# Kernel optimization log

Measured on AMD Instinct MI355X. Metric: run time of the kernel, lower is better.

Reference implementation:

```python
import jax, jax.numpy as jnp
import numpy as np


def setup_inputs() -> dict:
    key = jax.random.key(0)
    kq, kk, kv = jax.random.split(key, 3)
    B, S, D = 4, 4096, 64
    q = jax.random.normal(kq, (B, S, D), dtype=jnp.float32)
    k = jax.random.normal(kk, (B, S, D), dtype=jnp.float32)
    v = jax.random.normal(kv, (B, S, D), dtype=jnp.float32)
    return {"q": q, "k": k, "v": v}


def reference(q, k, v):
    # Faithful math of the original blocked loop:
    #   output_i += exp(Q_i @ K_j^T) @ V_j, summed over all column blocks j
    # which is exactly unnormalized exponential attention:
    #   out = exp(Q K^T) V  (no 1/sqrt(d) scaling, no softmax normalization,
    #   no max-subtraction -- matching the source module's math).
    scores = jnp.einsum("bqd,bkd->bqk", q, k)  # [B, Sq, Sk]
    return jnp.einsum("bqk,bkd->bqd", jnp.exp(scores), v)  # [B, Sq, D]
```

## Files before the change

### kernel.cpp

```cpp
#include <hip/hip_runtime.h>
#include <hip/hip_bf16.h>


typedef short    s16x4 __attribute__((ext_vector_type(4)));
typedef short    s16x8 __attribute__((ext_vector_type(8)));
typedef _Float16 h16x8 __attribute__((ext_vector_type(8)));
typedef float    fx4   __attribute__((ext_vector_type(4)));
typedef float    fx16  __attribute__((ext_vector_type(16)));

constexpr int S = 4096, D = 64, BN = 128;
constexpr int QROWS = 128;
constexpr int TILES = S / BN;
constexpr int HALF_TILES = TILES / 2;
constexpr int TILE_SHORTS  = 16 * 512;
constexpr int BATCH_SHORTS = TILES * TILE_SHORTS;

__device__ __forceinline__ unsigned short f2bf(float x) {
    unsigned u = __float_as_uint(x);
    u = (u + 0x7FFFu + ((u >> 16) & 1u)) >> 16;
    return (unsigned short)u;
}
__device__ __forceinline__ float bf2f(unsigned short h) {
    return __uint_as_float(((unsigned)h) << 16);
}
__device__ __forceinline__ unsigned short f2h(float x) {
    union { _Float16 h; unsigned short s; } u;
    u.h = (_Float16)x;
    return u.s;
}
__device__ __forceinline__ unsigned pack_bf16(float lo, float hi) {
    __hip_bfloat162 r = __float22bfloat162_rn(make_float2(lo, hi));
    union { __hip_bfloat162 b; unsigned u; } c;
    c.b = r;
    return c.u;
}
__device__ __forceinline__ float ex2(float x) {
#if __has_builtin(__builtin_amdgcn_exp2f)
    return __builtin_amdgcn_exp2f(x);
#else
    return exp2f(x);
#endif
}

__global__ __launch_bounds__(256) void prep2(
    const float* __restrict__ k, const float* __restrict__ v,
    unsigned short* __restrict__ kf, unsigned short* __restrict__ vf)
{
    __shared__ unsigned short tile[128 * 72];
    const int tid   = threadIdx.x;
    const int which = blockIdx.x & 1;
    const int t     = (blockIdx.x >> 1) & 31;
    const int b     = blockIdx.x >> 6;
    const float* src = (which ? v : k) + ((size_t)b * S + t * BN) * D;

    #pragma unroll
    for (int i = 0; i < 8; ++i) {
        int f   = i * 256 + tid;
        int row = f >> 4;
        int c4  = (f & 15) << 2;
        float4 x = *(const float4*)(src + row * D + c4);
        s16x4 o;
        if (which) o = (s16x4){(short)f2bf(x.x), (short)f2bf(x.y),
                               (short)f2bf(x.z), (short)f2bf(x.w)};
        else       o = (s16x4){(short)f2h(x.x), (short)f2h(x.y),
                               (short)f2h(x.z), (short)f2h(x.w)};
        *(s16x4*)&tile[row * 72 + c4] = o;
    }
    __syncthreads();

    const int lane = tid & 63;
    unsigned short* dst = (which ? vf : kf) + (size_t)b * BATCH_SHORTS + t * TILE_SHORTS;
    #pragma unroll
    for (int i = 0; i < 4; ++i) {
        int c = (tid >> 6) * 4 + i;
        s16x8 o;
        if (which == 0) {
            int row = (c >> 2) * 32 + (lane & 31);
            int dc  = (c & 3) * 16 + (lane >> 5) * 8;
            o = *(const s16x8*)&tile[row * 72 + dc];
        } else {
            int r0 = (c >> 1) * 16 + (lane >> 5) * 8;
            int dc = (c & 1) * 32 + (lane & 31);
            #pragma unroll
            for (int j = 0; j < 8; ++j) o[j] = (short)tile[(r0 + j) * 72 + dc];
        }
        *(s16x8*)(dst + c * 512 + lane * 8) = o;
    }
}

__global__ __launch_bounds__(512, 2) void attn_main4(
    const float* __restrict__ q, const unsigned short* __restrict__ kf,
    const unsigned short* __restrict__ vf, float* __restrict__ partial)
{
    __shared__ unsigned short smem[3 * 2 * TILE_SHORTS];

    const int tid = threadIdx.x, lane = tid & 63, w = tid >> 6;
    const int h = lane >> 5, m5 = lane & 31;
    const int mh = w & 1, kkq = w >> 1;
    const int bid = blockIdx.x;
    const int slice = bid & 7;
    const int b = slice >> 1;
    const int kh = slice & 1;
    const int q0 = (bid >> 3) * QROWS;
    const int t0 = kh * HALF_TILES;

    const unsigned short* kfb = kf + (size_t)b * BATCH_SHORTS;
    const unsigned short* vfb = vf + (size_t)b * BATCH_SHORTS;

    const float LOG2E = 1.4426950408889634f;
    h16x8 qf[2][4];
    #pragma unroll
    for (int mt = 0; mt < 2; ++mt) {
        const float* qrow = q + ((size_t)b * S + q0 + mh * 64 + mt * 32 + m5) * D + h * 8;
        #pragma unroll
        for (int ks = 0; ks < 4; ++ks) {
            float4 a = *(const float4*)(qrow + ks * 16);
            float4 c = *(const float4*)(qrow + ks * 16 + 4);
            qf[mt][ks] = (h16x8){
                (_Float16)(a.x * LOG2E), (_Float16)(a.y * LOG2E),
                (_Float16)(a.z * LOG2E), (_Float16)(a.w * LOG2E),
                (_Float16)(c.x * LOG2E), (_Float16)(c.y * LOG2E),
                (_Float16)(c.z * LOG2E), (_Float16)(c.w * LOG2E)};
        }
    }

    fx16 oacc[2][2] = {};

    auto issue = [&](int t, int bi) {
        unsigned short* base = &smem[bi * 2 * TILE_SHORTS];
        #pragma unroll
        for (int ii = 0; ii < 4; ++ii) {
            int c = (ii & 1) * 8 + w;
            const unsigned short* g = (ii < 2 ? kfb : vfb)
                + (size_t)t * TILE_SHORTS + c * 512 + lane * 8;
            unsigned short* l = base + (ii < 2 ? 0 : TILE_SHORTS) + c * 512 + lane * 8;
            __builtin_amdgcn_global_load_lds(
                (const __attribute__((address_space(1))) unsigned int*)g,
                (__attribute__((address_space(3))) unsigned int*)l, 16, 0, 0);
        }
    };

    issue(t0 + 0, 0);
    issue(t0 + 1, 1);

    for (int i = 0; i < HALF_TILES; ++i) {
        const int bi = i % 3;
        __asm__ volatile("" ::: "memory");
        if (i + 1 < HALF_TILES) {
            __builtin_amdgcn_s_waitcnt(0x0F74);
        } else {
            __builtin_amdgcn_s_waitcnt(0x0F70);
        }
        __builtin_amdgcn_s_barrier();
        __asm__ volatile("" ::: "memory");
        if (i + 2 < HALF_TILES) issue(t0 + i + 2, (i + 2) % 3);

        const unsigned short* kb = &smem[bi * 2 * TILE_SHORTS];
        const unsigned short* vb = kb + TILE_SHORTS;

        fx16 sa[2] = {};
        #pragma unroll
        for (int ks = 0; ks < 4; ++ks) {
            h16x8 a = *(const h16x8*)(kb + (kkq * 4 + ks) * 512 + lane * 8);
            #pragma unroll
            for (int mt = 0; mt < 2; ++mt)
                sa[mt] = __builtin_amdgcn_mfma_f32_32x32x16_f16(a, qf[mt][ks], sa[mt], 0, 0, 0);
        }

        unsigned p01[2][8];
        #pragma unroll
        for (int mt = 0; mt < 2; ++mt)
            #pragma unroll
            for (int rp = 0; rp < 8; ++rp)
                p01[mt][rp] = pack_bf16(ex2(sa[mt][2 * rp]), ex2(sa[mt][2 * rp + 1]));

        union frag { unsigned u[4]; s16x8 v; };
        frag A[2][2];
        #pragma unroll
        for (int mt = 0; mt < 2; ++mt) {
#if __has_builtin(__builtin_amdgcn_permlane32_swap)
            typedef unsigned uix2 __attribute__((ext_vector_type(2)));
            uix2 r0 = __builtin_amdgcn_permlane32_swap(p01[mt][0], p01[mt][2], false, false);
            uix2 r1 = __builtin_amdgcn_permlane32_swap(p01[mt][1], p01[mt][3], false, false);
            A[mt][0].u[0] = r0.x; A[mt][0].u[1] = r1.x;
            A[mt][0].u[2] = r0.y; A[mt][0].u[3] = r1.y;
            uix2 r2 = __builtin_amdgcn_permlane32_swap(p01[mt][4], p01[mt][6], false, false);
            uix2 r3 = __builtin_amdgcn_permlane32_swap(p01[mt][5], p01[mt][7], false, false);
            A[mt][1].u[0] = r2.x; A[mt][1].u[1] = r3.x;
            A[mt][1].u[2] = r2.y; A[mt][1].u[3] = r3.y;
#else
            unsigned sw[8];
            #pragma unroll
            for (int rp = 0; rp < 8; ++rp)
                sw[rp] = (unsigned)__shfl_xor((int)p01[mt][rp], 32, 64);
            A[mt][0].u[0] = h ? sw[2]        : p01[mt][0];
            A[mt][0].u[1] = h ? sw[3]        : p01[mt][1];
            A[mt][0].u[2] = h ? p01[mt][2]   : sw[0];
            A[mt][0].u[3] = h ? p01[mt][3]   : sw[1];
            A[mt][1].u[0] = h ? sw[6]        : p01[mt][4];
            A[mt][1].u[1] = h ? sw[7]        : p01[mt][5];
            A[mt][1].u[2] = h ? p01[mt][6]   : sw[4];
            A[mt][1].u[3] = h ? p01[mt][7]   : sw[5];
#endif
        }

        #pragma unroll
        for (int u = 0; u < 2; ++u) {
            int ss = kkq * 2 + u;
            #pragma unroll
            for (int dt = 0; dt < 2; ++dt) {
                s16x8 vv = *(const s16x8*)(vb + (ss * 2 + dt) * 512 + lane * 8);
                #pragma unroll
                for (int mt = 0; mt < 2; ++mt)
                    oacc[mt][dt] = __builtin_amdgcn_mfma_f32_32x32x16_bf16(
                        A[mt][u].v, vv, oacc[mt][dt], 0, 0, 0);
            }
        }
    }

    __syncthreads();
    float* scratch = (float*)smem;
    float* pout = partial + ((size_t)kh * 4 + b) * S * D;
    #pragma unroll
    for (int dt = 0; dt < 2; ++dt) {
        if (kkq > 0) {
            float* dst = scratch + (size_t)(mh * 3 + (kkq - 1)) * 2048;
            #pragma unroll
            for (int mt = 0; mt < 2; ++mt)
                #pragma unroll
                for (int r = 0; r < 16; ++r)
                    dst[(mt * 16 + r) * 64 + lane] = oacc[mt][dt][r];
        }
        __syncthreads();
        if (kkq == 0) {
            #pragma unroll
            for (int mt = 0; mt < 2; ++mt)
                #pragma unroll
                for (int r = 0; r < 16; ++r) {
                    float val = oacc[mt][dt][r];
                    #pragma unroll
                    for (int p = 0; p < 3; ++p)
                        val += scratch[(size_t)(mh * 3 + p) * 2048 + (mt * 16 + r) * 64 + lane];
                    int row = q0 + mh * 64 + mt * 32 + (r & 3) + 8 * (r >> 2) + 4 * h;
                    pout[(size_t)row * D + dt * 32 + m5] = val;
                }
        }
        __syncthreads();
    }
}

__global__ __launch_bounds__(256) void reduce_out(
    const float4* __restrict__ p0, const float4* __restrict__ p1,
    float4* __restrict__ o, int n4)
{
    int i = blockIdx.x * 256 + threadIdx.x;
    if (i < n4) {
        float4 a = p0[i], b = p1[i];
        o[i] = make_float4(a.x + b.x, a.y + b.y, a.z + b.z, a.w + b.w);
    }
}

__global__ __launch_bounds__(1024) void attn_fallback(
    const float* __restrict__ q, const float* __restrict__ k,
    const float* __restrict__ v, float* __restrict__ out)
{
    __shared__ unsigned short Kh[64][72];
    __shared__ unsigned short Kl[64][72];
    __shared__ unsigned short Vt[64][68];
    __shared__ unsigned short Pf[64][72];

    const int tid = threadIdx.x, lane = tid & 63, wave = tid >> 6;
    const int quad = lane >> 4, tq = lane & 15;
    const int kkb = wave & 3, mba = wave >> 2;
    const int b = blockIdx.y, q0 = blockIdx.x * 64;
    const float* qb = q + (size_t)b * S * D;
    const float* kb = k + (size_t)b * S * D;
    const float* vb = v + (size_t)b * S * D;
    float* ob = out + (size_t)b * S * D;

    s16x8 qh[2], ql[2];
    {
        const float* qrow = qb + (size_t)(q0 + mba * 16 + tq) * D;
        #pragma unroll
        for (int ks = 0; ks < 2; ++ks) {
            const float* src = qrow + ks * 32 + quad * 8;
            float4 f0 = *(const float4*)src;
            float4 f1 = *(const float4*)(src + 4);
            float f[8] = {f0.x, f0.y, f0.z, f0.w, f1.x, f1.y, f1.z, f1.w};
            #pragma unroll
            for (int j = 0; j < 8; ++j) {
                unsigned short hh = f2bf(f[j]);
                qh[ks][j] = (short)hh;
                ql[ks][j] = (short)f2bf(f[j] - bf2f(hh));
            }
        }
    }
    fx4 oacc = {0.f, 0.f, 0.f, 0.f};
    const int krow = tid >> 4, kc4 = (tid & 15) << 2;
    const int vd = tid & 63, vk = (tid >> 6) << 2;

    for (int t = 0; t < S / 64; ++t) {
        __syncthreads();
        const float* kt = kb + (size_t)(t * 64 + krow) * D;
        const float* vt = vb + (size_t)(t * 64 + vk) * D;
        {
            float4 kv = *(const float4*)(kt + kc4);
            unsigned short h0 = f2bf(kv.x), h1 = f2bf(kv.y), h2 = f2bf(kv.z), h3 = f2bf(kv.w);
            s16x4 a = {(short)h0, (short)h1, (short)h2, (short)h3};
            s16x4 l4 = {(short)f2bf(kv.x - bf2f(h0)), (short)f2bf(kv.y - bf2f(h1)),
                        (short)f2bf(kv.z - bf2f(h2)), (short)f2bf(kv.w - bf2f(h3))};
            *(s16x4*)&Kh[krow][kc4] = a;
            *(s16x4*)&Kl[krow][kc4] = l4;
            const float* vs = vt + vd;
            s16x4 vv = {(short)f2bf(vs[0]), (short)f2bf(vs[D]),
                        (short)f2bf(vs[2 * D]), (short)f2bf(vs[3 * D])};
            *(s16x4*)&Vt[vd][vk] = vv;
        }
        __syncthreads();
        fx4 sacc = {0.f, 0.f, 0.f, 0.f};
        #pragma unroll
        for (int ks = 0; ks < 2; ++ks) {
            s16x8 kah = *(const s16x8*)&Kh[kkb * 16 + tq][ks * 32 + quad * 8];
            s16x8 kal = *(const s16x8*)&Kl[kkb * 16 + tq][ks * 32 + quad * 8];
            sacc = __builtin_amdgcn_mfma_f32_16x16x32_bf16(kah, qh[ks], sacc, 0, 0, 0);
            sacc = __builtin_amdgcn_mfma_f32_16x16x32_bf16(kah, ql[ks], sacc, 0, 0, 0);
            sacc = __builtin_amdgcn_mfma_f32_16x16x32_bf16(kal, qh[ks], sacc, 0, 0, 0);
        }
        s16x4 pp = {(short)f2bf(__expf(sacc[0])), (short)f2bf(__expf(sacc[1])),
                    (short)f2bf(__expf(sacc[2])), (short)f2bf(__expf(sacc[3]))};
        *(s16x4*)&Pf[mba * 16 + tq][kkb * 16 + (quad << 2)] = pp;
        __syncthreads();
        #pragma unroll
        for (int ks = 0; ks < 2; ++ks) {
            s16x8 pa = *(const s16x8*)&Pf[mba * 16 + tq][ks * 32 + quad * 8];
            const unsigned short* vr = &Vt[kkb * 16 + tq][ks * 32 + quad * 8];
            s16x4 va = *(const s16x4*)vr;
            s16x4 vb2 = *(const s16x4*)(vr + 4);
            s16x8 vfull = __builtin_shufflevector(va, vb2, 0, 1, 2, 3, 4, 5, 6, 7);
            oacc = __builtin_amdgcn_mfma_f32_16x16x32_bf16(pa, vfull, oacc, 0, 0, 0);
        }
    }
    #pragma unroll
    for (int r = 0; r < 4; ++r)
        ob[(size_t)(q0 + mba * 16 + quad * 4 + r) * D + kkb * 16 + tq] = oacc[r];
}

extern "C" void kernel_launch(void* const* d_in, const int* in_sizes, int n_in,
                              void* d_out, int out_size, void* d_ws, size_t ws_size,
                              hipStream_t stream) {
    const float* q = (const float*)d_in[0];
    const float* k = (const float*)d_in[1];
    const float* v = (const float*)d_in[2];
    float* out = (float*)d_out;
    const int nbatch = in_sizes[0] / (S * D);
    const size_t elems = (size_t)nbatch * S * D;

    const size_t need = elems * 2 * 2 + elems * 2 * 4;
    if (nbatch == 4 && ws_size >= need && d_ws != nullptr) {
        unsigned short* kf = (unsigned short*)d_ws;
        unsigned short* vf = kf + elems;
        float* partial = (float*)(vf + elems);

        prep2<<<nbatch * TILES * 2, 256, 0, stream>>>(k, v, kf, vf);
        attn_main4<<<256, 512, 0, stream>>>(q, kf, vf, partial);
        const int n4 = (int)(elems / 4);
        reduce_out<<<(n4 + 255) / 256, 256, 0, stream>>>(
            (const float4*)partial, (const float4*)(partial + elems),
            (float4*)out, n4);
    } else {
        dim3 grid(S / 64, nbatch);
        attn_fallback<<<grid, 1024, 0, stream>>>(q, k, v, out);
    }
}
```

Before: 95.96 us.

## Fuse K/V prep, attention and reduction into one cooperative kernel

Replaces the three-kernel pipeline (prep, attention, partial reduce) with a single cooperative kernel. It zeroes the output, converts K/V tiles, grid-syncs, then runs the attention loop and accumulates the two key-half partials directly into the output with atomicAdd. This removes two kernel launches and the partial-buffer round trip. In exchange it adds a grid-wide barrier, float atomics (non-deterministic summation order), and a dependency on cooperative launch succeeding, with the old path kept as a fallback.

```diff
diff --git a/kernel.cpp b/kernel.cpp
--- a/kernel.cpp
+++ b/kernel.cpp
@@ -1,5 +1,8 @@
 #include <hip/hip_runtime.h>
+#include <hip/hip_cooperative_groups.h>
 #include <hip/hip_bf16.h>
+
+namespace cg = cooperative_groups;
 
 
 typedef short    s16x4 __attribute__((ext_vector_type(4)));
@@ -40,6 +43,219 @@
 #else
     return exp2f(x);
 #endif
+}
+
+__global__ __launch_bounds__(512, 2) void attn_fused(
+    const float* __restrict__ q, const float* __restrict__ k,
+    const float* __restrict__ v, unsigned short* __restrict__ kf,
+    unsigned short* __restrict__ vf, float* __restrict__ out)
+{
+    __shared__ unsigned short smem[3 * 2 * TILE_SHORTS];
+
+    const int tid = threadIdx.x;
+    const int bid = blockIdx.x;
+
+    {
+        float4 z = make_float4(0.f, 0.f, 0.f, 0.f);
+        float4* oz = (float4*)out + (size_t)bid * 1024 + tid;
+        oz[0] = z;
+        oz[512] = z;
+
+        const int which = bid & 1;
+        const int t     = (bid >> 1) & 31;
+        const int b     = bid >> 6;
+        const float* src = (which ? v : k) + ((size_t)b * S + t * BN) * D;
+        unsigned short* tile = smem;
+
+        #pragma unroll
+        for (int i = 0; i < 4; ++i) {
+            int f   = i * 512 + tid;
+            int row = f >> 4;
+            int c4  = (f & 15) << 2;
+            float4 x = *(const float4*)(src + row * D + c4);
+            s16x4 o;
+            if (which) o = (s16x4){(short)f2bf(x.x), (short)f2bf(x.y),
+                                   (short)f2bf(x.z), (short)f2bf(x.w)};
+            else       o = (s16x4){(short)f2h(x.x), (short)f2h(x.y),
+                                   (short)f2h(x.z), (short)f2h(x.w)};
+            *(s16x4*)&tile[row * 72 + c4] = o;
+        }
+        __syncthreads();
+
+        const int lane = tid & 63;
+        unsigned short* dst = (which ? vf : kf) + (size_t)b * BATCH_SHORTS + t * TILE_SHORTS;
+        #pragma unroll
+        for (int i = 0; i < 2; ++i) {
+            int c = (tid >> 6) * 2 + i;
+            s16x8 o;
+            if (which == 0) {
+                int row = (c >> 2) * 32 + (lane & 31);
+                int dc  = (c & 3) * 16 + (lane >> 5) * 8;
+                o = *(const s16x8*)&tile[row * 72 + dc];
+            } else {
+                int r0 = (c >> 1) * 16 + (lane >> 5) * 8;
+                int dc = (c & 1) * 32 + (lane & 31);
+                #pragma unroll
+                for (int j = 0; j < 8; ++j) o[j] = (short)tile[(r0 + j) * 72 + dc];
+            }
+            *(s16x8*)(dst + c * 512 + lane * 8) = o;
+        }
+    }
+
+    cg::this_grid().sync();
+
+    const int lane = tid & 63, w = tid >> 6;
+    const int h = lane >> 5, m5 = lane & 31;
+    const int mh = w & 1, kkq = w >> 1;
+    const int slice = bid & 7;
+    const int b = slice >> 1;
+    const int kh = slice & 1;
+    const int q0 = (bid >> 3) * QROWS;
+    const int t0 = kh * HALF_TILES;
+
+    const unsigned short* kfb = kf + (size_t)b * BATCH_SHORTS;
+    const unsigned short* vfb = vf + (size_t)b * BATCH_SHORTS;
+
+    const float LOG2E = 1.4426950408889634f;
+    h16x8 qf[2][4];
+    #pragma unroll
+    for (int mt = 0; mt < 2; ++mt) {
+        const float* qrow = q + ((size_t)b * S + q0 + mh * 64 + mt * 32 + m5) * D + h * 8;
+        #pragma unroll
+        for (int ks = 0; ks < 4; ++ks) {
+            float4 a = *(const float4*)(qrow + ks * 16);
+            float4 c = *(const float4*)(qrow + ks * 16 + 4);
+            qf[mt][ks] = (h16x8){
+                (_Float16)(a.x * LOG2E), (_Float16)(a.y * LOG2E),
+                (_Float16)(a.z * LOG2E), (_Float16)(a.w * LOG2E),
+                (_Float16)(c.x * LOG2E), (_Float16)(c.y * LOG2E),
+                (_Float16)(c.z * LOG2E), (_Float16)(c.w * LOG2E)};
+        }
+    }
+
+    fx16 oacc[2][2] = {};
+
+    auto issue = [&](int t, int bi) {
+        unsigned short* base = &smem[bi * 2 * TILE_SHORTS];
+        #pragma unroll
+        for (int ii = 0; ii < 4; ++ii) {
+            int c = (ii & 1) * 8 + w;
+            const unsigned short* g = (ii < 2 ? kfb : vfb)
+                + (size_t)t * TILE_SHORTS + c * 512 + lane * 8;
+            unsigned short* l = base + (ii < 2 ? 0 : TILE_SHORTS) + c * 512 + lane * 8;
+            __builtin_amdgcn_global_load_lds(
+                (const __attribute__((address_space(1))) unsigned int*)g,
+                (__attribute__((address_space(3))) unsigned int*)l, 16, 0, 0);
+        }
+    };
+
+    issue(t0 + 0, 0);
+    issue(t0 + 1, 1);
+
+    for (int i = 0; i < HALF_TILES; ++i) {
+        const int bi = i % 3;
+        __asm__ volatile("" ::: "memory");
+        if (i + 1 < HALF_TILES) {
+            __builtin_amdgcn_s_waitcnt(0x0F74);
+        } else {
+            __builtin_amdgcn_s_waitcnt(0x0F70);
+        }
+        __builtin_amdgcn_s_barrier();
+        __asm__ volatile("" ::: "memory");
+        if (i + 2 < HALF_TILES) issue(t0 + i + 2, (i + 2) % 3);
+
+        const unsigned short* kb = &smem[bi * 2 * TILE_SHORTS];
+        const unsigned short* vb = kb + TILE_SHORTS;
+
+        fx16 sa[2] = {};
+        #pragma unroll
+        for (int ks = 0; ks < 4; ++ks) {
+            h16x8 a = *(const h16x8*)(kb + (kkq * 4 + ks) * 512 + lane * 8);
+            #pragma unroll
+            for (int mt = 0; mt < 2; ++mt)
+                sa[mt] = __builtin_amdgcn_mfma_f32_32x32x16_f16(a, qf[mt][ks], sa[mt], 0, 0, 0);
+        }
+
+        unsigned p01[2][8];
+        #pragma unroll
+        for (int mt = 0; mt < 2; ++mt)
+            #pragma unroll
+            for (int rp = 0; rp < 8; ++rp)
+                p01[mt][rp] = pack_bf16(ex2(sa[mt][2 * rp]), ex2(sa[mt][2 * rp + 1]));
+
+        union frag { unsigned u[4]; s16x8 v; };
+        frag A[2][2];
+        #pragma unroll
+        for (int mt = 0; mt < 2; ++mt) {
+#if __has_builtin(__builtin_amdgcn_permlane32_swap)
+            typedef unsigned uix2 __attribute__((ext_vector_type(2)));
+            uix2 r0 = __builtin_amdgcn_permlane32_swap(p01[mt][0], p01[mt][2], false, false);
+            uix2 r1 = __builtin_amdgcn_permlane32_swap(p01[mt][1], p01[mt][3], false, false);
+            A[mt][0].u[0] = r0.x; A[mt][0].u[1] = r1.x;
+            A[mt][0].u[2] = r0.y; A[mt][0].u[3] = r1.y;
+            uix2 r2 = __builtin_amdgcn_permlane32_swap(p01[mt][4], p01[mt][6], false, false);
+            uix2 r3 = __builtin_amdgcn_permlane32_swap(p01[mt][5], p01[mt][7], false, false);
+            A[mt][1].u[0] = r2.x; A[mt][1].u[1] = r3.x;
+            A[mt][1].u[2] = r2.y; A[mt][1].u[3] = r3.y;
+#else
+            unsigned sw[8];
+            #pragma unroll
+            for (int rp = 0; rp < 8; ++rp)
+                sw[rp] = (unsigned)__shfl_xor((int)p01[mt][rp], 32, 64);
+            A[mt][0].u[0] = h ? sw[2]        : p01[mt][0];
+            A[mt][0].u[1] = h ? sw[3]        : p01[mt][1];
+            A[mt][0].u[2] = h ? p01[mt][2]   : sw[0];
+            A[mt][0].u[3] = h ? p01[mt][3]   : sw[1];
+            A[mt][1].u[0] = h ? sw[6]        : p01[mt][4];
+            A[mt][1].u[1] = h ? sw[7]        : p01[mt][5];
+            A[mt][1].u[2] = h ? p01[mt][6]   : sw[4];
+            A[mt][1].u[3] = h ? p01[mt][7]   : sw[5];
+#endif
+        }
+
+        #pragma unroll
+        for (int u = 0; u < 2; ++u) {
+            int ss = kkq * 2 + u;
+            #pragma unroll
+            for (int dt = 0; dt < 2; ++dt) {
+                s16x8 vv = *(const s16x8*)(vb + (ss * 2 + dt) * 512 + lane * 8);
+                #pragma unroll
+                for (int mt = 0; mt < 2; ++mt)
+                    oacc[mt][dt] = __builtin_amdgcn_mfma_f32_32x32x16_bf16(
+                        A[mt][u].v, vv, oacc[mt][dt], 0, 0, 0);
+            }
+        }
+    }
+
+    __syncthreads();
+    float* scratch = (float*)smem;
+    float* ob = out + (size_t)b * S * D;
+    #pragma unroll
+    for (int dt = 0; dt < 2; ++dt) {
+        if (kkq > 0) {
+            float* dst = scratch + (size_t)(mh * 3 + (kkq - 1)) * 2048;
+            #pragma unroll
+            for (int mt = 0; mt < 2; ++mt)
+                #pragma unroll
+                for (int r = 0; r < 16; ++r)
+                    dst[(mt * 16 + r) * 64 + lane] = oacc[mt][dt][r];
+        }
+        __syncthreads();
+        if (kkq == 0) {
+            #pragma unroll
+            for (int mt = 0; mt < 2; ++mt)
+                #pragma unroll
+                for (int r = 0; r < 16; ++r) {
+                    float val = oacc[mt][dt][r];
+                    #pragma unroll
+                    for (int p = 0; p < 3; ++p)
+                        val += scratch[(size_t)(mh * 3 + p) * 2048 + (mt * 16 + r) * 64 + lane];
+                    int row = q0 + mh * 64 + mt * 32 + (r & 3) + 8 * (r >> 2) + 4 * h;
+                    atomicAdd(&ob[(size_t)row * D + dt * 32 + m5], val);
+                }
+        }
+        __syncthreads();
+    }
 }
 
 __global__ __launch_bounds__(256) void prep2(
@@ -361,12 +577,20 @@
         unsigned short* vf = kf + elems;
         float* partial = (float*)(vf + elems);
 
-        prep2<<<nbatch * TILES * 2, 256, 0, stream>>>(k, v, kf, vf);
-        attn_main4<<<256, 512, 0, stream>>>(q, kf, vf, partial);
-        const int n4 = (int)(elems / 4);
-        reduce_out<<<(n4 + 255) / 256, 256, 0, stream>>>(
-            (const float4*)partial, (const float4*)(partial + elems),
-            (float4*)out, n4);
+        const float* qa = q; const float* ka = k; const float* va = v;
+        unsigned short* kfa = kf; unsigned short* vfa = vf; float* outa = out;
+        void* args[] = {(void*)&qa, (void*)&ka, (void*)&va,
+                        (void*)&kfa, (void*)&vfa, (void*)&outa};
+        hipError_t err = hipLaunchCooperativeKernel(
+            (void*)attn_fused, dim3(256), dim3(512), args, 0, stream);
+        if (err != hipSuccess) {
+            prep2<<<nbatch * TILES * 2, 256, 0, stream>>>(k, v, kf, vf);
+            attn_main4<<<256, 512, 0, stream>>>(q, kf, vf, partial);
+            const int n4 = (int)(elems / 4);
+            reduce_out<<<(n4 + 255) / 256, 256, 0, stream>>>(
+                (const float4*)partial, (const float4*)(partial + elems),
+                (float4*)out, n4);
+        }
     } else {
         dim3 grid(S / 64, nbatch);
         attn_fallback<<<grid, 1024, 0, stream>>>(q, k, v, out);
```

Measured after the change: 141.2 us. 1.47x slower.

## Split attention into single-wave blocks with 8-way partial sums and global reduction

Applied to the files above, without the earlier changes.

Replaces the 512-thread attention blocks, which reduced their 4 key-chunk waves through shared memory, with 2048 single-wave blocks. Each block handles 64 query rows and one quarter of every key tile, writes its own partial output, and relies on an 8-way reduce kernel to sum them. The block barrier and shared-memory reduction go away, and staging drops to double-buffered per-wave slices. In exchange the partial-sum buffer and reduction traffic grow fourfold, and Q fragments are reloaded by more blocks.

```diff
diff --git a/kernel.cpp b/kernel.cpp
--- a/kernel.cpp
+++ b/kernel.cpp
@@ -9,7 +9,6 @@
 typedef float    fx16  __attribute__((ext_vector_type(16)));
 
 constexpr int S = 4096, D = 64, BN = 128;
-constexpr int QROWS = 128;
 constexpr int TILES = S / BN;
 constexpr int HALF_TILES = TILES / 2;
 constexpr int TILE_SHORTS  = 16 * 512;
@@ -88,20 +87,21 @@
     }
 }
 
-__global__ __launch_bounds__(512, 2) void attn_main4(
+__global__ __launch_bounds__(64) void attn_main8(
     const float* __restrict__ q, const unsigned short* __restrict__ kf,
     const unsigned short* __restrict__ vf, float* __restrict__ partial)
 {
-    __shared__ unsigned short smem[3 * 2 * TILE_SHORTS];
-
-    const int tid = threadIdx.x, lane = tid & 63, w = tid >> 6;
+    __shared__ unsigned short smem[2 * 8 * 512];
+
+    const int lane = threadIdx.x;
     const int h = lane >> 5, m5 = lane & 31;
-    const int mh = w & 1, kkq = w >> 1;
     const int bid = blockIdx.x;
     const int slice = bid & 7;
     const int b = slice >> 1;
     const int kh = slice & 1;
-    const int q0 = (bid >> 3) * QROWS;
+    const int idx = bid >> 3;
+    const int kkq = idx & 3;
+    const int q0 = (idx >> 2) * 64;
     const int t0 = kh * HALF_TILES;
 
     const unsigned short* kfb = kf + (size_t)b * BATCH_SHORTS;
@@ -111,7 +111,7 @@
     h16x8 qf[2][4];
     #pragma unroll
     for (int mt = 0; mt < 2; ++mt) {
-        const float* qrow = q + ((size_t)b * S + q0 + mh * 64 + mt * 32 + m5) * D + h * 8;
+        const float* qrow = q + ((size_t)b * S + q0 + mt * 32 + m5) * D + h * 8;
         #pragma unroll
         for (int ks = 0; ks < 4; ++ks) {
             float4 a = *(const float4*)(qrow + ks * 16);
@@ -127,13 +127,13 @@
     fx16 oacc[2][2] = {};
 
     auto issue = [&](int t, int bi) {
-        unsigned short* base = &smem[bi * 2 * TILE_SHORTS];
-        #pragma unroll
-        for (int ii = 0; ii < 4; ++ii) {
-            int c = (ii & 1) * 8 + w;
-            const unsigned short* g = (ii < 2 ? kfb : vfb)
+        unsigned short* base = &smem[bi * 8 * 512];
+        #pragma unroll
+        for (int ii = 0; ii < 8; ++ii) {
+            int c = kkq * 4 + (ii & 3);
+            const unsigned short* g = (ii < 4 ? kfb : vfb)
                 + (size_t)t * TILE_SHORTS + c * 512 + lane * 8;
-            unsigned short* l = base + (ii < 2 ? 0 : TILE_SHORTS) + c * 512 + lane * 8;
+            unsigned short* l = base + ii * 512 + lane * 8;
             __builtin_amdgcn_global_load_lds(
                 (const __attribute__((address_space(1))) unsigned int*)g,
                 (__attribute__((address_space(3))) unsigned int*)l, 16, 0, 0);
@@ -144,24 +144,22 @@
     issue(t0 + 1, 1);
 
     for (int i = 0; i < HALF_TILES; ++i) {
-        const int bi = i % 3;
+        const int bi = i & 1;
         __asm__ volatile("" ::: "memory");
         if (i + 1 < HALF_TILES) {
-            __builtin_amdgcn_s_waitcnt(0x0F74);
+            __builtin_amdgcn_s_waitcnt(0x0F78);
         } else {
             __builtin_amdgcn_s_waitcnt(0x0F70);
         }
-        __builtin_amdgcn_s_barrier();
         __asm__ volatile("" ::: "memory");
-        if (i + 2 < HALF_TILES) issue(t0 + i + 2, (i + 2) % 3);
-
-        const unsigned short* kb = &smem[bi * 2 * TILE_SHORTS];
-        const unsigned short* vb = kb + TILE_SHORTS;
+
+        const unsigned short* kb = &smem[bi * 8 * 512];
+        const unsigned short* vb = kb + 4 * 512;
 
         fx16 sa[2] = {};
         #pragma unroll
         for (int ks = 0; ks < 4; ++ks) {
-            h16x8 a = *(const h16x8*)(kb + (kkq * 4 + ks) * 512 + lane * 8);
+            h16x8 a = *(const h16x8*)(kb + ks * 512 + lane * 8);
             #pragma unroll
             for (int mt = 0; mt < 2; ++mt)
                 sa[mt] = __builtin_amdgcn_mfma_f32_32x32x16_f16(a, qf[mt][ks], sa[mt], 0, 0, 0);
@@ -206,57 +204,43 @@
 
         #pragma unroll
         for (int u = 0; u < 2; ++u) {
-            int ss = kkq * 2 + u;
             #pragma unroll
             for (int dt = 0; dt < 2; ++dt) {
-                s16x8 vv = *(const s16x8*)(vb + (ss * 2 + dt) * 512 + lane * 8);
+                s16x8 vv = *(const s16x8*)(vb + (u * 2 + dt) * 512 + lane * 8);
                 #pragma unroll
                 for (int mt = 0; mt < 2; ++mt)
                     oacc[mt][dt] = __builtin_amdgcn_mfma_f32_32x32x16_bf16(
                         A[mt][u].v, vv, oacc[mt][dt], 0, 0, 0);
             }
         }
-    }
-
-    __syncthreads();
-    float* scratch = (float*)smem;
-    float* pout = partial + ((size_t)kh * 4 + b) * S * D;
-    #pragma unroll
-    for (int dt = 0; dt < 2; ++dt) {
-        if (kkq > 0) {
-            float* dst = scratch + (size_t)(mh * 3 + (kkq - 1)) * 2048;
-            #pragma unroll
-            for (int mt = 0; mt < 2; ++mt)
-                #pragma unroll
-                for (int r = 0; r < 16; ++r)
-                    dst[(mt * 16 + r) * 64 + lane] = oacc[mt][dt][r];
-        }
-        __syncthreads();
-        if (kkq == 0) {
-            #pragma unroll
-            for (int mt = 0; mt < 2; ++mt)
-                #pragma unroll
-                for (int r = 0; r < 16; ++r) {
-                    float val = oacc[mt][dt][r];
-                    #pragma unroll
-                    for (int p = 0; p < 3; ++p)
-                        val += scratch[(size_t)(mh * 3 + p) * 2048 + (mt * 16 + r) * 64 + lane];
-                    int row = q0 + mh * 64 + mt * 32 + (r & 3) + 8 * (r >> 2) + 4 * h;
-                    pout[(size_t)row * D + dt * 32 + m5] = val;
-                }
-        }
-        __syncthreads();
-    }
-}
-
-__global__ __launch_bounds__(256) void reduce_out(
-    const float4* __restrict__ p0, const float4* __restrict__ p1,
-    float4* __restrict__ o, int n4)
+
+        if (i + 2 < HALF_TILES) issue(t0 + i + 2, bi);
+    }
+
+    float* pout = partial + (((size_t)(kh * 4 + kkq)) * 4 + b) * S * D;
+    #pragma unroll
+    for (int dt = 0; dt < 2; ++dt)
+        #pragma unroll
+        for (int mt = 0; mt < 2; ++mt)
+            #pragma unroll
+            for (int r = 0; r < 16; ++r) {
+                int row = q0 + mt * 32 + (r & 3) + 8 * (r >> 2) + 4 * h;
+                pout[(size_t)row * D + dt * 32 + m5] = oacc[mt][dt][r];
+            }
+}
+
+__global__ __launch_bounds__(256) void reduce_out8(
+    const float4* __restrict__ p, float4* __restrict__ o, int n4)
 {
     int i = blockIdx.x * 256 + threadIdx.x;
     if (i < n4) {
-        float4 a = p0[i], b = p1[i];
-        o[i] = make_float4(a.x + b.x, a.y + b.y, a.z + b.z, a.w + b.w);
+        float4 a = p[i];
+        #pragma unroll
+        for (int j = 1; j < 8; ++j) {
+            float4 x = p[(size_t)j * n4 + i];
+            a.x += x.x; a.y += x.y; a.z += x.z; a.w += x.w;
+        }
+        o[i] = a;
     }
 }
 
@@ -355,18 +339,17 @@
     const int nbatch = in_sizes[0] / (S * D);
     const size_t elems = (size_t)nbatch * S * D;
 
-    const size_t need = elems * 2 * 2 + elems * 2 * 4;
+    const size_t need = elems * 2 * 2 + elems * 8 * 4;
     if (nbatch == 4 && ws_size >= need && d_ws != nullptr) {
         unsigned short* kf = (unsigned short*)d_ws;
         unsigned short* vf = kf + elems;
         float* partial = (float*)(vf + elems);
 
         prep2<<<nbatch * TILES * 2, 256, 0, stream>>>(k, v, kf, vf);
-        attn_main4<<<256, 512, 0, stream>>>(q, kf, vf, partial);
+        attn_main8<<<2048, 64, 0, stream>>>(q, kf, vf, partial);
         const int n4 = (int)(elems / 4);
-        reduce_out<<<(n4 + 255) / 256, 256, 0, stream>>>(
-            (const float4*)partial, (const float4*)(partial + elems),
-            (float4*)out, n4);
+        reduce_out8<<<(n4 + 255) / 256, 256, 0, stream>>>(
+            (const float4*)partial, (float4*)out, n4);
     } else {
         dim3 grid(S / 64, nbatch);
         attn_fallback<<<grid, 1024, 0, stream>>>(q, k, v, out);
```

Result: slower. 99.69 us (+3.9%).
